# Kernel tuning notes

Measured on AMD Instinct MI355X. Metric: run time of the kernel, lower is better.

Reference implementation:

```python
import jax, jax.numpy as jnp
import numpy as np

EMBED_DIM = 256
N_HEADS = 8
N_LEVELS = 4
N_POINTS = 4
BATCH = 2
LEVEL_SHAPES = np.array([[64, 64], [32, 32], [16, 16], [8, 8]], dtype=np.int32)


def setup_inputs() -> dict:
    key = jax.random.key(0)
    ks = jax.random.split(key, 12)
    tok_per_img = int((LEVEL_SHAPES[:, 0] * LEVEL_SHAPES[:, 1]).sum())  # 5440
    n_q = BATCH * tok_per_img  # 10880
    level_spatial_shapes = jnp.asarray(LEVEL_SHAPES, jnp.int32)
    # queries are multi-level tokens, laid out level-by-level per image
    lvl = np.concatenate([np.full(int(h * w), l, np.int32) for l, (h, w) in enumerate(LEVEL_SHAPES)])
    query_level_indices = jnp.asarray(np.tile(lvl, BATCH), jnp.int32)
    query = jax.random.normal(ks[0], (n_q, EMBED_DIM), jnp.float32)
    pos01 = jax.random.uniform(ks[1], (n_q, 2), jnp.float32)
    query_spatial_positions = pos01 * level_spatial_shapes[query_level_indices].astype(jnp.float32)
    query_batch_offsets = jnp.asarray([i * tok_per_img for i in range(BATCH + 1)], jnp.int32)
    Hm, Wm = int(LEVEL_SHAPES[:, 0].max()), int(LEVEL_SHAPES[:, 1].max())
    feature_maps = jax.random.normal(ks[2], (BATCH, Hm, Wm, N_LEVELS, EMBED_DIM), jnp.float32)
    s = 0.02
    W_off = jax.random.normal(ks[3], (EMBED_DIM, N_POINTS * N_LEVELS * N_HEADS * 2), jnp.float32) * s
    b_off = jax.random.normal(ks[4], (N_POINTS * N_LEVELS * N_HEADS * 2,), jnp.float32)
    W_attn = jax.random.normal(ks[5], (EMBED_DIM, N_POINTS * N_LEVELS * N_HEADS), jnp.float32) * s
    b_attn = jnp.zeros((N_POINTS * N_LEVELS * N_HEADS,), jnp.float32)
    W_val = jax.random.normal(ks[6], (EMBED_DIM, EMBED_DIM), jnp.float32) * s
    b_val = jnp.zeros((EMBED_DIM,), jnp.float32)
    W_out = jax.random.normal(ks[7], (EMBED_DIM, EMBED_DIM), jnp.float32) * s
    b_out = jnp.zeros((EMBED_DIM,), jnp.float32)
    return {"query": query, "query_spatial_positions": query_spatial_positions,
            "query_batch_offsets": query_batch_offsets, "feature_maps": feature_maps,
            "level_spatial_shapes": level_spatial_shapes, "query_level_indices": query_level_indices,
            "W_off": W_off, "b_off": b_off, "W_attn": W_attn, "b_attn": b_attn,
            "W_val": W_val, "b_val": b_val, "W_out": W_out, "b_out": b_out}


def reference(query, query_spatial_positions, query_batch_offsets, feature_maps,
              level_spatial_shapes, query_level_indices,
              W_off, b_off, W_attn, b_attn, W_val, b_val, W_out, b_out):
    n_q = query.shape[0]
    B, Hm, Wm, L, D = feature_maps.shape
    H, P = N_HEADS, N_POINTS
    hd = D // H
    shapes_f = level_spatial_shapes.astype(query.dtype)  # [L,2]

    # Sparse tensor semantics: level l only has specified entries on its [H_l, W_l] grid;
    # value_proj is applied to specified values only, unspecified entries stay zero.
    hh = jnp.arange(Hm)[:, None, None]
    ww = jnp.arange(Wm)[None, :, None]
    valid = (hh < level_spatial_shapes[None, None, :, 0]) & (ww < level_spatial_shapes[None, None, :, 1])  # [Hm,Wm,L]
    values = (feature_maps @ W_val + b_val) * valid[None, :, :, :, None].astype(query.dtype)
    values = values.reshape(B, Hm, Wm, L, H, hd)  # split heads

    off = (query @ W_off + b_off).reshape(n_q, P, L, H, 2)
    attw = (query @ W_attn + b_attn).reshape(n_q, P * L, H)
    attw = jax.nn.softmax(attw, axis=-2).reshape(n_q, P, L, H)

    # rescale each query position to every level's coordinate system
    norm = query_spatial_positions / shapes_f[query_level_indices]  # [n_q,2]
    scaled = norm[:, None, :] * shapes_f  # [n_q,L,2]
    loc = scaled[:, None, :, None, :] + off  # [n_q,P,L,H,2]
    loc = jnp.clip(loc, 0.0, shapes_f[:, None, :])  # clamp to [0, level_shape]

    b_idx = jnp.searchsorted(query_batch_offsets, jnp.arange(n_q), side="right") - 1  # [n_q]

    h = loc[..., 0]
    w = loc[..., 1]
    h0 = jnp.floor(h)
    w0 = jnp.floor(w)
    fh = h - h0
    fw = w - w0
    h0i = h0.astype(jnp.int32)
    w0i = w0.astype(jnp.int32)

    Hl = level_spatial_shapes[None, None, :, None, 0]  # [1,1,L,1]
    Wl = level_spatial_shapes[None, None, :, None, 1]
    b_b = b_idx[:, None, None, None]
    l_b = jnp.arange(L)[None, None, :, None]
    head_b = jnp.arange(H)[None, None, None, :]

    def gather(hi, wi):
        # out-of-level-range lookups hit unspecified entries -> zero
        ok = (hi >= 0) & (hi < Hl) & (wi >= 0) & (wi < Wl)
        hi_c = jnp.clip(hi, 0, Hm - 1)
        wi_c = jnp.clip(wi, 0, Wm - 1)
        v = values[b_b, hi_c, wi_c, l_b, head_b]  # [n_q,P,L,H,hd]
        return v * ok[..., None].astype(v.dtype)

    sampled = (gather(h0i, w0i) * ((1 - fh) * (1 - fw))[..., None]
               + gather(h0i, w0i + 1) * ((1 - fh) * fw)[..., None]
               + gather(h0i + 1, w0i) * (fh * (1 - fw))[..., None]
               + gather(h0i + 1, w0i + 1) * (fh * fw)[..., None])  # [n_q,P,L,H,hd]

    out = jnp.einsum("qplhd,qplh->qhd", sampled, attw).reshape(n_q, D)
    return out @ W_out + b_out
```

## Files before the change

### kernel.cpp

```cpp
#include <hip/hip_runtime.h>
#include <hip/hip_bf16.h>
#include <math.h>

#define NQ   10880
#define TOK  5440

typedef short s16x8 __attribute__((ext_vector_type(8)));
typedef float f32x4 __attribute__((ext_vector_type(4)));

__device__ __forceinline__ float bf2f_lo(unsigned int u) {
    return __uint_as_float(u << 16);
}
__device__ __forceinline__ float bf2f_hi(unsigned int u) {
    return __uint_as_float(u & 0xFFFF0000u);
}
__device__ __forceinline__ unsigned short f2bf(float f) {
    unsigned int u = __float_as_uint(f);
    u += 0x7FFFu + ((u >> 16) & 1u);
    return (unsigned short)(u >> 16);
}
__device__ __forceinline__ unsigned int pack2(float a, float b) {
    __hip_bfloat162 h = __float22bfloat162_rn(make_float2(a, b));
    return *reinterpret_cast<unsigned int*>(&h);
}

__global__ __launch_bounds__(256) void prepW_k(
    const float* __restrict__ W_val, const float* __restrict__ W_off,
    const float* __restrict__ W_attn, const float* __restrict__ W_out,
    unsigned short* __restrict__ WtAll)
{
    __shared__ unsigned short T[64][72];
    const int bt = blockIdx.x;
    const int tid = threadIdx.x;
    const int kt = bt & 3;
    const int ct = bt >> 2;
    const int c0 = ct * 64;
    const float* Wp; int ldw, cl0;
    if (c0 < 256)      { Wp = W_val;  ldw = 256; cl0 = c0; }
    else if (c0 < 512) { Wp = W_off;  ldw = 256; cl0 = c0 - 256; }
    else if (c0 < 640) { Wp = W_attn; ldw = 128; cl0 = c0 - 512; }
    else               { Wp = W_out;  ldw = 256; cl0 = c0 - 640; }

    const int kk = tid >> 2;
    const int cq = (tid & 3) << 4;
    const float* src = Wp + (size_t)(kt * 64 + kk) * ldw + cl0 + cq;
    float4 f0 = *(const float4*)(src);
    float4 f1 = *(const float4*)(src + 4);
    float4 f2 = *(const float4*)(src + 8);
    float4 f3 = *(const float4*)(src + 12);
    uint4 w0, w1;
    w0.x = pack2(f0.x, f0.y); w0.y = pack2(f0.z, f0.w);
    w0.z = pack2(f1.x, f1.y); w0.w = pack2(f1.z, f1.w);
    w1.x = pack2(f2.x, f2.y); w1.y = pack2(f2.z, f2.w);
    w1.z = pack2(f3.x, f3.y); w1.w = pack2(f3.z, f3.w);
    *(uint4*)&T[kk][cq]     = w0;
    *(uint4*)&T[kk][cq + 8] = w1;
    __syncthreads();
    const int cc = tid >> 2;
    const int kq = (tid & 3) << 4;
    union { unsigned short u[16]; uint4 q[2]; } ob;
#pragma unroll
    for (int j = 0; j < 16; ++j) ob.u[j] = T[kq + j][cc];
    unsigned short* dst = WtAll + (size_t)(c0 + cc) * 256 + kt * 64 + kq;
    *(uint4*)(dst)     = ob.q[0];
    *(uint4*)(dst + 8) = ob.q[1];
}

__global__ __launch_bounds__(256) void gemm_fused_k(
    const float* __restrict__ query, const float* __restrict__ fm,
    const unsigned short* __restrict__ qoutbf,
    const unsigned short* __restrict__ Wt,
    const float* __restrict__ b_val, const float* __restrict__ b_off,
    const float* __restrict__ b_attn, const float* __restrict__ b_out,
    unsigned short* __restrict__ values, float* __restrict__ offattn,
    float* __restrict__ out, int mode)
{
    __shared__ unsigned short As[64][72];
    __shared__ unsigned short Bs[128][72];

    const int tid = threadIdx.x;
    const int bm = blockIdx.x, bn = blockIdx.y;

    const float* bias;
    void* Cp; int ldc, col0, cbf, wr0;
    if (mode == 0) {
        if (bn < 2) {
            wr0 = bn * 128; bias = b_val + bn * 128;
            Cp = values; ldc = 256; col0 = bn * 128; cbf = 1;
        } else {
            wr0 = bn * 128;
            bias = (bn == 4) ? b_attn : b_off + (bn - 2) * 128;
            Cp = offattn; ldc = 384; col0 = (bn - 2) * 128; cbf = 0;
        }
    } else {
        wr0 = 640 + bn * 128; bias = b_out + bn * 128;
        Cp = out; ldc = 256; col0 = bn * 128; cbf = 0;
    }

    const int asrc = (mode == 1) ? 2 : ((bn < 2) ? 0 : 1);
    const int arow = tid >> 2;
    const int ac   = (tid & 3) << 4;
    const int r    = bm * 64 + arow;
    const float* a32 = nullptr;
    const unsigned short* a16 = nullptr;
    if (asrc == 0) {
        const int b = (r >= TOK) ? 1 : 0;
        const int t = r - b * TOK;
        int l, hh, ww;
        if (t < 4096)      { l = 0; hh = t >> 6; ww = t & 63; }
        else if (t < 5120) { int i = t - 4096; l = 1; hh = i >> 5; ww = i & 31; }
        else if (t < 5376) { int i = t - 5120; l = 2; hh = i >> 4; ww = i & 15; }
        else               { int i = t - 5376; l = 3; hh = i >> 3; ww = i & 7; }
        a32 = fm + ((size_t)((((b * 64 + hh) * 64 + ww) * 4) + l) << 8) + ac;
    } else if (asrc == 1) {
        a32 = query + (size_t)r * 256 + ac;
    } else {
        a16 = qoutbf + (size_t)r * 256 + ac;
    }

    const int brow = tid >> 1;
    const int bc   = (tid & 1) << 5;
    const unsigned short* Bp = Wt + (size_t)(wr0 + brow) * 256 + bc;

    const int w = tid >> 6, lane = tid & 63;
    const int quad = lane >> 4, fl = lane & 15;
    const int quad8 = quad << 3;
    const int mW = (w >> 1) << 5;
    const int nW = (w & 1) << 6;

    f32x4 acc[2][4] = {};

    for (int k0 = 0; k0 < 256; k0 += 64) {
        uint4 av0, av1;
        if (a16) {
            av0 = *(const uint4*)(a16 + k0);
            av1 = *(const uint4*)(a16 + k0 + 8);
        } else {
            const float* s = a32 + k0;
            float4 f0 = *(const float4*)(s);
            float4 f1 = *(const float4*)(s + 4);
            float4 f2 = *(const float4*)(s + 8);
            float4 f3 = *(const float4*)(s + 12);
            av0.x = pack2(f0.x, f0.y); av0.y = pack2(f0.z, f0.w);
            av0.z = pack2(f1.x, f1.y); av0.w = pack2(f1.z, f1.w);
            av1.x = pack2(f2.x, f2.y); av1.y = pack2(f2.z, f2.w);
            av1.z = pack2(f3.x, f3.y); av1.w = pack2(f3.z, f3.w);
        }
        uint4 bv0 = *(const uint4*)(Bp + k0);
        uint4 bv1 = *(const uint4*)(Bp + k0 + 8);
        uint4 bv2 = *(const uint4*)(Bp + k0 + 16);
        uint4 bv3 = *(const uint4*)(Bp + k0 + 24);
        __syncthreads();
        *(uint4*)&As[arow][ac]     = av0;
        *(uint4*)&As[arow][ac + 8] = av1;
        *(uint4*)&Bs[brow][bc]      = bv0;
        *(uint4*)&Bs[brow][bc + 8]  = bv1;
        *(uint4*)&Bs[brow][bc + 16] = bv2;
        *(uint4*)&Bs[brow][bc + 24] = bv3;
        __syncthreads();
#pragma unroll
        for (int ks = 0; ks < 64; ks += 32) {
            s16x8 af[2], bf[4];
#pragma unroll
            for (int i = 0; i < 2; ++i)
                af[i] = *(const s16x8*)&As[mW + i * 16 + fl][ks + quad8];
#pragma unroll
            for (int j = 0; j < 4; ++j)
                bf[j] = *(const s16x8*)&Bs[nW + j * 16 + fl][ks + quad8];
#pragma unroll
            for (int i = 0; i < 2; ++i)
#pragma unroll
                for (int j = 0; j < 4; ++j)
                    acc[i][j] = __builtin_amdgcn_mfma_f32_16x16x32_bf16(
                        af[i], bf[j], acc[i][j], 0, 0, 0);
        }
    }

    float* Cf = (float*)Cp;
    unsigned short* Cb = (unsigned short*)Cp;
#pragma unroll
    for (int j = 0; j < 4; ++j) {
        const int c = nW + j * 16 + fl;
        const float bv = bias[c];
        const int cg = col0 + c;
#pragma unroll
        for (int i = 0; i < 2; ++i) {
            const int row0 = bm * 64 + mW + i * 16 + (quad << 2);
#pragma unroll
            for (int rr = 0; rr < 4; ++rr) {
                const float v = acc[i][j][rr] + bv;
                if (cbf) Cb[(size_t)(row0 + rr) * ldc + cg] = f2bf(v);
                else     Cf[(size_t)(row0 + rr) * ldc + cg] = v;
            }
        }
    }
}

__global__ __launch_bounds__(256) void sample_k(
    const float* __restrict__ offattn,
    const unsigned short* __restrict__ values,
    const float* __restrict__ qpos,
    const int*   __restrict__ qlevel,
    unsigned short* __restrict__ qout)
{
    __shared__ float  sRow[8][384];
    __shared__ float4 sW[8][128];
    __shared__ int4   sIdx[8][128];

    const int tid = threadIdx.x;

    const int band = blockIdx.x & 7;
    const int g    = blockIdx.x >> 3;
    const int bat  = g / 85;
    const int i0   = (g % 85) << 3;
    int qs;
    if (i0 < 512)      qs = band * 512 + i0;
    else if (i0 < 640) qs = 4096 + band * 128 + (i0 - 512);
    else if (i0 < 672) qs = 5120 + band * 32 + (i0 - 640);
    else               qs = 5376 + band * 8;
    const int qbase = bat * TOK + qs;

    {
        const float4* rb = (const float4*)(offattn + (size_t)qbase * 384);
        float4* sf = (float4*)sRow;
#pragma unroll
        for (int i = 0; i < 3; ++i) sf[tid + i * 256] = rb[tid + i * 256];
    }
    __syncthreads();

    if (tid < 64) {
        const int qn = tid >> 3, h = tid & 7;
        float m = -1e30f;
#pragma unroll
        for (int j = 0; j < 16; ++j) m = fmaxf(m, sRow[qn][256 + j * 8 + h]);
        float e[16], s = 0.f;
#pragma unroll
        for (int j = 0; j < 16; ++j) { e[j] = __expf(sRow[qn][256 + j * 8 + h] - m); s += e[j]; }
        float inv = 1.0f / s;
#pragma unroll
        for (int j = 0; j < 16; ++j) sRow[qn][256 + j * 8 + h] = e[j] * inv;
    }
    __syncthreads();

    const int LBASE[4] = {0, 4096, 5120, 5376};
#pragma unroll
    for (int ss = 0; ss < 4; ++ss) {
        const int s  = tid + ss * 256;
        const int qn = s >> 7;
        const int c  = s & 127;
        const int pl = c >> 3;
        const int l  = pl & 3;
        const int q  = qbase + qn;
        const int b  = (q >= TOK) ? 1 : 0;
        const float ph = qpos[2 * q], pw = qpos[2 * q + 1];
        const int ql = qlevel[q];
        const float invq = 1.0f / (float)(64 >> ql);
        const int Hl = 64 >> l;
        const float Hlf = (float)Hl;
        const float sc = invq * Hlf;
        float lh = ph * sc + sRow[qn][2 * c];
        float lw = pw * sc + sRow[qn][2 * c + 1];
        const float aw = sRow[qn][256 + c];
        lh = fminf(fmaxf(lh, 0.f), Hlf);
        lw = fminf(fmaxf(lw, 0.f), Hlf);
        const float fh0 = floorf(lh), fw0 = floorf(lw);
        const int h0 = (int)fh0, w0 = (int)fw0;
        const float fh = lh - fh0, fw = lw - fw0;
        float w00 = (1.f - fh) * (1.f - fw);
        float w01 = (1.f - fh) * fw;
        float w10 = fh * (1.f - fw);
        float w11 = fh * fw;
        if (h0     >= Hl) { w00 = 0.f; w01 = 0.f; }
        if (h0 + 1 >= Hl) { w10 = 0.f; w11 = 0.f; }
        if (w0     >= Hl) { w00 = 0.f; w10 = 0.f; }
        if (w0 + 1 >= Hl) { w01 = 0.f; w11 = 0.f; }
        const int h0c = min(h0, Hl - 1), h1c = min(h0 + 1, Hl - 1);
        const int w0c = min(w0, Hl - 1), w1c = min(w0 + 1, Hl - 1);
        const int base = b * TOK + LBASE[l];
        sW[qn][c]   = make_float4(aw * w00, aw * w01, aw * w10, aw * w11);
        sIdx[qn][c] = make_int4((base + h0c * Hl + w0c) << 8,
                                (base + h0c * Hl + w1c) << 8,
                                (base + h1c * Hl + w0c) << 8,
                                (base + h1c * Hl + w1c) << 8);
    }
    __syncthreads();

    const int qn = tid >> 5;
    const int t  = tid & 31;
    const int h  = t >> 2;
    const int dg = t & 3;
    const unsigned short* vb = values + h * 32 + (dg << 3);
    float a[8] = {};
#pragma unroll
    for (int pl = 0; pl < 16; ++pl) {
        const int c = pl * 8 + h;
        const float4 wt = sW[qn][c];
        const int4  id = sIdx[qn][c];
        const uint4 u00 = *(const uint4*)(vb + id.x);
        const uint4 u01 = *(const uint4*)(vb + id.y);
        const uint4 u10 = *(const uint4*)(vb + id.z);
        const uint4 u11 = *(const uint4*)(vb + id.w);
#define ACC8(U, W)                                         \
        a[0] = fmaf(W, bf2f_lo(U.x), a[0]);                \
        a[1] = fmaf(W, bf2f_hi(U.x), a[1]);                \
        a[2] = fmaf(W, bf2f_lo(U.y), a[2]);                \
        a[3] = fmaf(W, bf2f_hi(U.y), a[3]);                \
        a[4] = fmaf(W, bf2f_lo(U.z), a[4]);                \
        a[5] = fmaf(W, bf2f_hi(U.z), a[5]);                \
        a[6] = fmaf(W, bf2f_lo(U.w), a[6]);                \
        a[7] = fmaf(W, bf2f_hi(U.w), a[7]);
        ACC8(u00, wt.x)
        ACC8(u01, wt.y)
        ACC8(u10, wt.z)
        ACC8(u11, wt.w)
#undef ACC8
    }
    const int q = qbase + qn;
    uint4 o;
    o.x = pack2(a[0], a[1]);
    o.y = pack2(a[2], a[3]);
    o.z = pack2(a[4], a[5]);
    o.w = pack2(a[6], a[7]);
    *(uint4*)(qout + (size_t)q * 256 + h * 32 + (dg << 3)) = o;
}

extern "C" void kernel_launch(void* const* d_in, const int* in_sizes, int n_in,
                              void* d_out, int out_size, void* d_ws, size_t ws_size,
                              hipStream_t stream)
{
    const float* query  = (const float*)d_in[0];
    const float* qpos   = (const float*)d_in[1];
    const float* fm     = (const float*)d_in[3];
    const int*   qlvl   = (const int*)d_in[5];
    const float* W_off  = (const float*)d_in[6];
    const float* b_off  = (const float*)d_in[7];
    const float* W_attn = (const float*)d_in[8];
    const float* b_attn = (const float*)d_in[9];
    const float* W_val  = (const float*)d_in[10];
    const float* b_val  = (const float*)d_in[11];
    const float* W_out  = (const float*)d_in[12];
    const float* b_out  = (const float*)d_in[13];
    float* out = (float*)d_out;

    char* ws = (char*)d_ws;
    unsigned short* WtAll   = (unsigned short*)ws;
    unsigned short* values  = WtAll + (size_t)896 * 256;
    unsigned short* qout    = values + (size_t)NQ * 256;
    float*          offattn = (float*)(qout + (size_t)NQ * 256);

    dim3 blk(256);
    prepW_k<<<dim3(56), blk, 0, stream>>>(W_val, W_off, W_attn, W_out, WtAll);
    gemm_fused_k<<<dim3(170, 5), blk, 0, stream>>>(query, fm, nullptr, WtAll,
                                                   b_val, b_off, b_attn, b_out,
                                                   values, offattn, out, 0);
    sample_k<<<dim3(NQ / 8), blk, 0, stream>>>(offattn, values, qpos, qlvl, qout);
    gemm_fused_k<<<dim3(170, 2), blk, 0, stream>>>(query, fm, qout, WtAll,
                                                   b_val, b_off, b_attn, b_out,
                                                   values, offattn, out, 1);
}
```

Before: 154.9 us.

## Fuse output projection GEMM into sampling kernel via per-block MFMA

Removes the separate output-projection GEMM launch by computing out = sampled·W_out + b in the sampling kernel, staging the 8 sampled query rows in LDS (padded to 16 with zeros) and running bf16 MFMAs against W_out read directly from global memory. This eliminates the bf16 intermediate write/read and one kernel launch. In exchange every block re-reads the whole W_out matrix from cache, and half of each MFMA tile is wasted on zero padding.

```diff
diff --git a/kernel.cpp b/kernel.cpp
--- a/kernel.cpp
+++ b/kernel.cpp
@@ -68,12 +68,10 @@
 
 __global__ __launch_bounds__(256) void gemm_fused_k(
     const float* __restrict__ query, const float* __restrict__ fm,
-    const unsigned short* __restrict__ qoutbf,
     const unsigned short* __restrict__ Wt,
     const float* __restrict__ b_val, const float* __restrict__ b_off,
-    const float* __restrict__ b_attn, const float* __restrict__ b_out,
-    unsigned short* __restrict__ values, float* __restrict__ offattn,
-    float* __restrict__ out, int mode)
+    const float* __restrict__ b_attn,
+    unsigned short* __restrict__ values, float* __restrict__ offattn)
 {
     __shared__ unsigned short As[64][72];
     __shared__ unsigned short Bs[128][72];
@@ -83,27 +81,20 @@
 
     const float* bias;
     void* Cp; int ldc, col0, cbf, wr0;
-    if (mode == 0) {
-        if (bn < 2) {
-            wr0 = bn * 128; bias = b_val + bn * 128;
-            Cp = values; ldc = 256; col0 = bn * 128; cbf = 1;
-        } else {
-            wr0 = bn * 128;
-            bias = (bn == 4) ? b_attn : b_off + (bn - 2) * 128;
-            Cp = offattn; ldc = 384; col0 = (bn - 2) * 128; cbf = 0;
-        }
+    if (bn < 2) {
+        wr0 = bn * 128; bias = b_val + bn * 128;
+        Cp = values; ldc = 256; col0 = bn * 128; cbf = 1;
     } else {
-        wr0 = 640 + bn * 128; bias = b_out + bn * 128;
-        Cp = out; ldc = 256; col0 = bn * 128; cbf = 0;
-    }
-
-    const int asrc = (mode == 1) ? 2 : ((bn < 2) ? 0 : 1);
+        wr0 = bn * 128;
+        bias = (bn == 4) ? b_attn : b_off + (bn - 2) * 128;
+        Cp = offattn; ldc = 384; col0 = (bn - 2) * 128; cbf = 0;
+    }
+
     const int arow = tid >> 2;
     const int ac   = (tid & 3) << 4;
     const int r    = bm * 64 + arow;
-    const float* a32 = nullptr;
-    const unsigned short* a16 = nullptr;
-    if (asrc == 0) {
+    const float* a32;
+    if (bn < 2) {
         const int b = (r >= TOK) ? 1 : 0;
         const int t = r - b * TOK;
         int l, hh, ww;
@@ -112,10 +103,8 @@
         else if (t < 5376) { int i = t - 5120; l = 2; hh = i >> 4; ww = i & 15; }
         else               { int i = t - 5376; l = 3; hh = i >> 3; ww = i & 7; }
         a32 = fm + ((size_t)((((b * 64 + hh) * 64 + ww) * 4) + l) << 8) + ac;
-    } else if (asrc == 1) {
+    } else {
         a32 = query + (size_t)r * 256 + ac;
-    } else {
-        a16 = qoutbf + (size_t)r * 256 + ac;
     }
 
     const int brow = tid >> 1;
@@ -132,10 +121,7 @@
 
     for (int k0 = 0; k0 < 256; k0 += 64) {
         uint4 av0, av1;
-        if (a16) {
-            av0 = *(const uint4*)(a16 + k0);
-            av1 = *(const uint4*)(a16 + k0 + 8);
-        } else {
+        {
             const float* s = a32 + k0;
             float4 f0 = *(const float4*)(s);
             float4 f1 = *(const float4*)(s + 4);
@@ -196,16 +182,19 @@
     }
 }
 
-__global__ __launch_bounds__(256) void sample_k(
+__global__ __launch_bounds__(256) void sampleout_k(
     const float* __restrict__ offattn,
     const unsigned short* __restrict__ values,
     const float* __restrict__ qpos,
     const int*   __restrict__ qlevel,
-    unsigned short* __restrict__ qout)
+    const unsigned short* __restrict__ WtAll,
+    const float* __restrict__ b_out,
+    float* __restrict__ out)
 {
     __shared__ float  sRow[8][384];
     __shared__ float4 sW[8][128];
     __shared__ int4   sIdx[8][128];
+    __shared__ unsigned short sQ[16][264];
 
     const int tid = threadIdx.x;
 
@@ -225,6 +214,12 @@
         float4* sf = (float4*)sRow;
 #pragma unroll
         for (int i = 0; i < 3; ++i) sf[tid + i * 256] = rb[tid + i * 256];
+    }
+    {
+        uint4 z = {0u, 0u, 0u, 0u};
+        uint4* zp = (uint4*)&sQ[8][0];
+        zp[tid] = z;
+        if (tid < 8) zp[256 + tid] = z;
     }
     __syncthreads();
 
@@ -285,43 +280,76 @@
     }
     __syncthreads();
 
-    const int qn = tid >> 5;
-    const int t  = tid & 31;
-    const int h  = t >> 2;
-    const int dg = t & 3;
-    const unsigned short* vb = values + h * 32 + (dg << 3);
-    float a[8] = {};
-#pragma unroll
-    for (int pl = 0; pl < 16; ++pl) {
-        const int c = pl * 8 + h;
-        const float4 wt = sW[qn][c];
-        const int4  id = sIdx[qn][c];
-        const uint4 u00 = *(const uint4*)(vb + id.x);
-        const uint4 u01 = *(const uint4*)(vb + id.y);
-        const uint4 u10 = *(const uint4*)(vb + id.z);
-        const uint4 u11 = *(const uint4*)(vb + id.w);
+    {
+        const int qn = tid >> 5;
+        const int t  = tid & 31;
+        const int h  = t >> 2;
+        const int dg = t & 3;
+        const unsigned short* vb = values + h * 32 + (dg << 3);
+        float a[8] = {};
+#pragma unroll
+        for (int pl = 0; pl < 16; ++pl) {
+            const int c = pl * 8 + h;
+            const float4 wt = sW[qn][c];
+            const int4  id = sIdx[qn][c];
+            const uint4 u00 = *(const uint4*)(vb + id.x);
+            const uint4 u01 = *(const uint4*)(vb + id.y);
+            const uint4 u10 = *(const uint4*)(vb + id.z);
+            const uint4 u11 = *(const uint4*)(vb + id.w);
 #define ACC8(U, W)                                         \
-        a[0] = fmaf(W, bf2f_lo(U.x), a[0]);                \
-        a[1] = fmaf(W, bf2f_hi(U.x), a[1]);                \
-        a[2] = fmaf(W, bf2f_lo(U.y), a[2]);                \
-        a[3] = fmaf(W, bf2f_hi(U.y), a[3]);                \
-        a[4] = fmaf(W, bf2f_lo(U.z), a[4]);                \
-        a[5] = fmaf(W, bf2f_hi(U.z), a[5]);                \
-        a[6] = fmaf(W, bf2f_lo(U.w), a[6]);                \
-        a[7] = fmaf(W, bf2f_hi(U.w), a[7]);
-        ACC8(u00, wt.x)
-        ACC8(u01, wt.y)
-        ACC8(u10, wt.z)
-        ACC8(u11, wt.w)
+            a[0] = fmaf(W, bf2f_lo(U.x), a[0]);            \
+            a[1] = fmaf(W, bf2f_hi(U.x), a[1]);            \
+            a[2] = fmaf(W, bf2f_lo(U.y), a[2]);            \
+            a[3] = fmaf(W, bf2f_hi(U.y), a[3]);            \
+            a[4] = fmaf(W, bf2f_lo(U.z), a[4]);            \
+            a[5] = fmaf(W, bf2f_hi(U.z), a[5]);            \
+            a[6] = fmaf(W, bf2f_lo(U.w), a[6]);            \
+            a[7] = fmaf(W, bf2f_hi(U.w), a[7]);
+            ACC8(u00, wt.x)
+            ACC8(u01, wt.y)
+            ACC8(u10, wt.z)
+            ACC8(u11, wt.w)
 #undef ACC8
-    }
-    const int q = qbase + qn;
-    uint4 o;
-    o.x = pack2(a[0], a[1]);
-    o.y = pack2(a[2], a[3]);
-    o.z = pack2(a[4], a[5]);
-    o.w = pack2(a[6], a[7]);
-    *(uint4*)(qout + (size_t)q * 256 + h * 32 + (dg << 3)) = o;
+        }
+        uint4 o;
+        o.x = pack2(a[0], a[1]);
+        o.y = pack2(a[2], a[3]);
+        o.z = pack2(a[4], a[5]);
+        o.w = pack2(a[6], a[7]);
+        *(uint4*)&sQ[qn][h * 32 + (dg << 3)] = o;
+    }
+    __syncthreads();
+
+    {
+        const int wv = tid >> 6, lane = tid & 63;
+        const int quad = lane >> 4, fl = lane & 15;
+        const int quad8 = quad << 3;
+        const unsigned short* Wo = WtAll + (size_t)(640 + wv * 64) * 256;
+        f32x4 oacc[4] = {};
+#pragma unroll
+        for (int kt = 0; kt < 8; ++kt) {
+            s16x8 afr = *(const s16x8*)&sQ[fl][kt * 32 + quad8];
+#pragma unroll
+            for (int nt = 0; nt < 4; ++nt) {
+                s16x8 bfr = *(const s16x8*)(Wo + (size_t)(nt * 16 + fl) * 256
+                                            + kt * 32 + quad8);
+                oacc[nt] = __builtin_amdgcn_mfma_f32_16x16x32_bf16(
+                    afr, bfr, oacc[nt], 0, 0, 0);
+            }
+        }
+        if (quad < 2) {
+#pragma unroll
+            for (int nt = 0; nt < 4; ++nt) {
+                const int cg = wv * 64 + nt * 16 + fl;
+                const float bv = b_out[cg];
+#pragma unroll
+                for (int rr = 0; rr < 4; ++rr) {
+                    const int q = qbase + (quad << 2) + rr;
+                    out[(size_t)q * 256 + cg] = oacc[nt][rr] + bv;
+                }
+            }
+        }
+    }
 }
 
 extern "C" void kernel_launch(void* const* d_in, const int* in_sizes, int n_in,
@@ -345,16 +373,13 @@
     char* ws = (char*)d_ws;
     unsigned short* WtAll   = (unsigned short*)ws;
     unsigned short* values  = WtAll + (size_t)896 * 256;
-    unsigned short* qout    = values + (size_t)NQ * 256;
-    float*          offattn = (float*)(qout + (size_t)NQ * 256);
+    float*          offattn = (float*)(values + (size_t)NQ * 256);
 
     dim3 blk(256);
     prepW_k<<<dim3(56), blk, 0, stream>>>(W_val, W_off, W_attn, W_out, WtAll);
-    gemm_fused_k<<<dim3(170, 5), blk, 0, stream>>>(query, fm, nullptr, WtAll,
-                                                   b_val, b_off, b_attn, b_out,
-                                                   values, offattn, out, 0);
-    sample_k<<<dim3(NQ / 8), blk, 0, stream>>>(offattn, values, qpos, qlvl, qout);
-    gemm_fused_k<<<dim3(170, 2), blk, 0, stream>>>(query, fm, qout, WtAll,
-                                                   b_val, b_off, b_attn, b_out,
-                                                   values, offattn, out, 1);
-}
+    gemm_fused_k<<<dim3(170, 5), blk, 0, stream>>>(query, fm, WtAll,
+                                                   b_val, b_off, b_attn,
+                                                   values, offattn);
+    sampleout_k<<<dim3(NQ / 8), blk, 0, stream>>>(offattn, values, qpos, qlvl,
+                                                  WtAll, b_out, out);
+}
```

Result: slower. 166.0 us (+7.1%).
